# Kernel tuning notes

Measured on AMD Instinct MI355X. Metric: run time of the kernel, lower is better.

Reference implementation:

```python
import jax, jax.numpy as jnp
import numpy as np

NN_SIZE = 10  # matches init_kwargs nn_size


def _knn_idx(points, k):
    """points: (B,N,D). Returns (B,N,k) indices of k nearest neighbors, self excluded."""
    sq = jnp.sum(points * points, axis=-1)  # (B,N)
    # squared euclidean distances (B,N,N)
    d2 = sq[:, :, None] + sq[:, None, :] - 2.0 * jnp.einsum('bnd,bmd->bnm', points, points)
    _, idx = jax.lax.top_k(-d2, k + 1)  # smallest distances; first hit is self
    return idx[:, :, 1:]  # drop self -> (B,N,k)


def _uniform_laplacian(points, knn_idx):
    """points: (B,N,D); knn_idx: (B,N,K). lap = mean(neighbors) - point."""
    neigh = jax.vmap(lambda p, i: p[i])(points, knn_idx)  # (B,N,K,D) gather per batch
    return jnp.mean(neigh, axis=2) - points


def setup_inputs() -> dict:
    key = jax.random.key(0)
    k1, k2 = jax.random.split(key)
    B, N, D = 2, 8192, 3
    point1 = jax.random.normal(k1, (B, N, D), dtype=jnp.float32)
    point2 = jax.random.normal(k2, (B, N, D), dtype=jnp.float32)
    return {"point1": point1, "point2": point2}


def reference(point1, point2):
    knn_idx = _knn_idx(point1, NN_SIZE)          # connectivity from ref cloud
    lap1 = _uniform_laplacian(point1, knn_idx)   # (B,N,3)
    lap2 = _uniform_laplacian(point2, knn_idx)   # reuse knn_idx
    # metric = L1Loss (mean reduction); use_norm=False
    return jnp.mean(jnp.abs(lap1 - lap2))
```

## Files before the change

### kernel.cpp

```cpp
#include <hip/hip_runtime.h>
#include <math.h>


constexpr int NPTS  = 8192;
constexpr int NB    = 2;
constexpr int KNN   = 10;
constexpr int QPB   = 64;
constexpr int WPB   = 8;
constexpr int BLOCK = QPB * WPB;
constexpr int MASK13 = 0xFFFFE000;

constexpr int   G    = 32;
constexpr int   NC   = G * G * G;
constexpr float BMIN = -5.5f;
constexpr float BW   = 11.0f;
constexpr float H    = BW / G;
constexpr float INVH = (float)G / BW;

__device__ __forceinline__ void ins1(int l[KNN], int x) {
#pragma unroll
    for (int k = KNN - 1; k > 0; --k) l[k] = min(l[k], max(l[k - 1], x));
    l[0] = min(l[0], x);
}
__device__ __forceinline__ void ins2(int l[KNN], int a, int b) {
    const int b0 = min(a, b), b1 = max(a, b);
#pragma unroll
    for (int k = KNN - 1; k >= 2; --k)
        l[k] = min(l[k], min(max(l[k - 1], b0), max(l[k - 2], b1)));
    l[1] = min(l[1], min(max(l[0], b0), b1));
    l[0] = min(l[0], b0);
}
template<int S>
__device__ __forceinline__ void ins2s(int l[KNN], int a, int b) {
    const int b0 = min(a, b), b1 = max(a, b);
#pragma unroll
    for (int k = KNN - 1; k >= S + 2; --k)
        l[k] = min(l[k], min(max(l[k - 1], b0), max(l[k - 2], b1)));
    l[S + 1] = min(l[S + 1], min(max(l[S], b0), b1));
    l[S] = min(l[S], b0);
}
__device__ __forceinline__ void merge_sorted(int l[KNN], const int p[KNN]) {
    ins2s<0>(l, p[0], p[1]);
    ins2s<2>(l, p[2], p[3]);
    ins2s<4>(l, p[4], p[5]);
    ins2s<6>(l, p[6], p[7]);
    ins2s<8>(l, p[8], p[9]);
}

__global__ void pack_bin(const float* __restrict__ p1, float4* __restrict__ w,
                         int* __restrict__ hist, int* __restrict__ cellof) {
    const int i = blockIdx.x * blockDim.x + threadIdx.x;
    if (i >= NB * NPTS) return;
    const float x = p1[3 * i], y = p1[3 * i + 1], z = p1[3 * i + 2];
    w[i] = make_float4(x, y, z, fmaf(x, x, fmaf(y, y, z * z)));
    const int cx = min(max((int)floorf((x - BMIN) * INVH), 0), G - 1);
    const int cy = min(max((int)floorf((y - BMIN) * INVH), 0), G - 1);
    const int cz = min(max((int)floorf((z - BMIN) * INVH), 0), G - 1);
    const int c = (cz << 10) | (cy << 5) | cx;
    cellof[i] = c;
    atomicAdd(&hist[(i >> 13) * NC + c], 1);
}

__global__ __launch_bounds__(1024)
void scan_cells(const int* __restrict__ hist, int* __restrict__ starts,
                float* __restrict__ out, int* __restrict__ nfail) {
    __shared__ int wsum[16];
    const int b = blockIdx.x, t = threadIdx.x;
    if (b == 0 && t == 0) { out[0] = 0.0f; nfail[0] = 0; }
    const int* hb = hist + b * NC;
    int* sb = starts + b * (NC + 1);
    const int c0 = t * 32;
    int loc[32]; int sum = 0;
#pragma unroll
    for (int j = 0; j < 32; ++j) { loc[j] = hb[c0 + j]; sum += loc[j]; }
    const int lane = t & 63, wv = t >> 6;
    int incl = sum;
#pragma unroll
    for (int off = 1; off < 64; off <<= 1) {
        const int v = __shfl_up(incl, off);
        if (lane >= off) incl += v;
    }
    if (lane == 63) wsum[wv] = incl;
    __syncthreads();
    if (t < 16) {
        const int v = wsum[t];
        int iv = v;
#pragma unroll
        for (int off = 1; off < 16; off <<= 1) {
            const int u = __shfl_up(iv, off);
            if (t >= off) iv += u;
        }
        wsum[t] = iv - v;
    }
    __syncthreads();
    int run = wsum[wv] + incl - sum;
#pragma unroll
    for (int j = 0; j < 32; ++j) { sb[c0 + j] = run; run += loc[j]; }
    if (t == 1023) sb[NC] = run;
}

__global__ void scatter_all(const int* __restrict__ cellof,
                            const int* __restrict__ starts,
                            int* __restrict__ hist,
                            const float4* __restrict__ w,
                            const float* __restrict__ p2,
                            float4* __restrict__ wsorted,
                            float4* __restrict__ p2s) {
    const int i = blockIdx.x * blockDim.x + threadIdx.x;
    if (i >= NB * NPTS) return;
    const int b = i >> 13;
    const int c = cellof[i];
    const int old = atomicSub(&hist[b * NC + c], 1);
    const int pos = b * NPTS + starts[b * (NC + 1) + c] + old - 1;
    wsorted[pos] = w[i];
    p2s[pos] = make_float4(p2[3 * i], p2[3 * i + 1], p2[3 * i + 2], 0.0f);
}

template<int S>
__device__ __forceinline__ void scan_neigh(const float4* __restrict__ W,
                                           const int* __restrict__ st,
                                           int cx, int cy, int cz,
                                           float m2x, float m2y, float m2z,
                                           float q2, int qpos, int wv,
                                           int l[KNN])
{
    const int IMAX = 0x7FFFFFFF;
    constexpr int Wd = 2 * S + 1;
#pragma unroll
    for (int r = 0; r < Wd * Wd; ++r) {
        const int dy = r % Wd - S, dz = r / Wd - S;
        const int ay = cy + dy, az = cz + dz;
        int j0 = 0, j1 = 0;
        if ((unsigned)ay < G && (unsigned)az < G) {
            const int cbase = (az << 10) | (ay << 5);
            j0 = st[cbase + max(cx - S, 0)];
            j1 = st[cbase + min(cx + S, G - 1) + 1];
        }
        for (int j = j0 + wv; j < j1; j += WPB) {
            const float4 c4 = W[j];
            const float d2 = fmaf(m2x, c4.x,
                             fmaf(m2y, c4.y,
                             fmaf(m2z, c4.z, c4.w + q2)));
            int key = (__float_as_int(d2) & MASK13) | j;
            key = (j == qpos) ? IMAX : key;
            ins1(l, key);
        }
    }
}

__global__ __launch_bounds__(BLOCK)
void phase1(const float4* __restrict__ wsorted, const float4* __restrict__ p2s,
            const int* __restrict__ starts, float* __restrict__ out,
            int* __restrict__ nfail, int* __restrict__ worklist)
{
    __shared__ int mv[WPB * KNN * QPB];

    const int batch = blockIdx.x >> 7;
    const int lane  = threadIdx.x & 63;
    const int wv    = __builtin_amdgcn_readfirstlane(threadIdx.x >> 6);
    const int qpos  = ((blockIdx.x & 127) << 6) + lane;

    const float4* W  = wsorted + batch * NPTS;
    const float4* P2 = p2s + batch * NPTS;
    const int*    st = starts + batch * (NC + 1);

    const float4 qp = W[qpos];
    const int cx = min(max((int)floorf((qp.x - BMIN) * INVH), 0), G - 1);
    const int cy = min(max((int)floorf((qp.y - BMIN) * INVH), 0), G - 1);
    const int cz = min(max((int)floorf((qp.z - BMIN) * INVH), 0), G - 1);
    const float lox = BMIN + cx * H, loy = BMIN + cy * H, loz = BMIN + cz * H;
    const float df = fminf(fminf(fminf(qp.x - lox, lox + H - qp.x),
                                 fminf(qp.y - loy, loy + H - qp.y)),
                           fminf(qp.z - loz, loz + H - qp.z));
    const float m2x = -2.0f * qp.x, m2y = -2.0f * qp.y, m2z = -2.0f * qp.z;
    const float q2 = qp.w;
    const int IMAX = 0x7FFFFFFF;

    const bool sparse = __any(q2 > 4.8f);
    const int s = sparse ? 2 : 1;

    int l[KNN];
#pragma unroll
    for (int k = 0; k < KNN; ++k) l[k] = IMAX;

    if (sparse)
        scan_neigh<2>(W, st, cx, cy, cz, m2x, m2y, m2z, q2, qpos, wv, l);
    else
        scan_neigh<1>(W, st, cx, cy, cz, m2x, m2y, m2z, q2, qpos, wv, l);

#pragma unroll
    for (int k = 0; k < KNN; ++k) mv[(wv * KNN + k) * QPB + lane] = l[k];
    __syncthreads();

    if (threadIdx.x < QPB) {
        int M[KNN];
#pragma unroll
        for (int k = 0; k < KNN; ++k) M[k] = IMAX;
#pragma unroll
        for (int e = 0; e < WPB; ++e) {
            int p[KNN];
#pragma unroll
            for (int k = 0; k < KNN; ++k) p[k] = mv[(e * KNN + k) * QPB + lane];
            merge_sorted(M, p);
        }

        const float tau = __int_as_float(M[KNN - 1] & MASK13);
        const float R = (float)s * H + df;
        const bool covered = (tau <= R * R * 0.996f);
        float v = 0.0f;
        if (covered) {
            float s1x = 0, s1y = 0, s1z = 0, s2x = 0, s2y = 0, s2z = 0;
#pragma unroll
            for (int k = 0; k < KNN; ++k) {
                const int j = M[k] & (NPTS - 1);
                const float4 c4 = W[j];
                const float4 n2 = P2[j];
                s1x += c4.x; s1y += c4.y; s1z += c4.z;
                s2x += n2.x; s2y += n2.y; s2z += n2.z;
            }
            const float4 p2v = P2[qpos];
            const float dx = (s1x * 0.1f - qp.x) - (s2x * 0.1f - p2v.x);
            const float dy2 = (s1y * 0.1f - qp.y) - (s2y * 0.1f - p2v.y);
            const float dz2 = (s1z * 0.1f - qp.z) - (s2z * 0.1f - p2v.z);
            v = fabsf(dx) + fabsf(dy2) + fabsf(dz2);
        } else {
            const int wi = atomicAdd(nfail, 1);
            worklist[wi] = (batch << 16) | qpos;
        }
#pragma unroll
        for (int off = 32; off >= 1; off >>= 1) v += __shfl_down(v, off);
        if (threadIdx.x == 0)
            atomicAdd(out, v * (1.0f / (float)(NB * NPTS * 3)));
    }
}

constexpr int P2BLK = 256;
constexpr int P2GRID = 512;

__global__ __launch_bounds__(P2BLK)
void phase2(const float4* __restrict__ wsorted, const float4* __restrict__ p2s,
            const int* __restrict__ nfail, const int* __restrict__ worklist,
            float* __restrict__ out)
{
    const int lane = threadIdx.x & 63;
    const int wv   = threadIdx.x >> 6;
    const int wid  = blockIdx.x * (P2BLK / 64) + wv;
    const int NW   = P2GRID * (P2BLK / 64);
    const int nf   = *nfail;
    const int IMAX = 0x7FFFFFFF;
    float acc = 0.0f;

    for (int i = wid; i < nf; i += NW) {
        const int e = worklist[i];
        const int batch = e >> 16, qpos = e & 0xFFFF;
        const float4* W  = wsorted + batch * NPTS;
        const float4* P2 = p2s + batch * NPTS;
        const float4 qp = W[qpos];
        const float m2x = -2.0f * qp.x, m2y = -2.0f * qp.y, m2z = -2.0f * qp.z;
        const float q2 = qp.w;

        int l[KNN];
#pragma unroll
        for (int k = 0; k < KNN; ++k) l[k] = IMAX;

#pragma unroll 2
        for (int it = 0; it < NPTS / 128; ++it) {
            const int ja = it * 128 + lane, jb = ja + 64;
            const float4 ca = W[ja];
            const float4 cb = W[jb];
            const float da = fmaf(m2x, ca.x, fmaf(m2y, ca.y, fmaf(m2z, ca.z, ca.w + q2)));
            const float db = fmaf(m2x, cb.x, fmaf(m2y, cb.y, fmaf(m2z, cb.z, cb.w + q2)));
            int ka = (__float_as_int(da) & MASK13) | ja;
            int kb = (__float_as_int(db) & MASK13) | jb;
            ka = (ja == qpos) ? IMAX : ka;
            kb = (jb == qpos) ? IMAX : kb;
            ins2(l, ka, kb);
        }
        for (int off = 1; off < 64; off <<= 1) {
            int p[KNN];
#pragma unroll
            for (int k = 0; k < KNN; ++k) p[k] = __shfl_xor(l[k], off);
            merge_sorted(l, p);
        }
        float s1x = 0, s1y = 0, s1z = 0, s2x = 0, s2y = 0, s2z = 0;
#pragma unroll
        for (int k = 0; k < KNN; ++k) {
            const int j = l[k] & (NPTS - 1);
            const float4 c4 = W[j];
            const float4 n2 = P2[j];
            s1x += c4.x; s1y += c4.y; s1z += c4.z;
            s2x += n2.x; s2y += n2.y; s2z += n2.z;
        }
        const float4 p2v = P2[qpos];
        const float dx = (s1x * 0.1f - qp.x) - (s2x * 0.1f - p2v.x);
        const float dy = (s1y * 0.1f - qp.y) - (s2y * 0.1f - p2v.y);
        const float dz = (s1z * 0.1f - qp.z) - (s2z * 0.1f - p2v.z);
        if (lane == 0) acc += fabsf(dx) + fabsf(dy) + fabsf(dz);
    }

    if (lane == 0 && acc != 0.0f)
        atomicAdd(out, acc * (1.0f / (float)(NB * NPTS * 3)));
}

constexpr int CHUNK = NPTS / WPB;

__global__ void prep_pack(const float* __restrict__ p, float4* __restrict__ w) {
    const int i = blockIdx.x * blockDim.x + threadIdx.x;
    if (i < NB * NPTS) {
        const float x = p[3 * i], y = p[3 * i + 1], z = p[3 * i + 2];
        w[i] = make_float4(x, y, z, fmaf(x, x, fmaf(y, y, z * z)));
    }
}

__global__ __launch_bounds__(BLOCK, 2)
void knn_lap(const float4* __restrict__ w1, const float* __restrict__ p2,
             float* __restrict__ out)
{
    __shared__ int mv[WPB * KNN * QPB];
    const int batch = blockIdx.x >> 7;
    const int qbase = (blockIdx.x & 127) << 6;
    const int lane  = threadIdx.x & 63;
    const int wv    = __builtin_amdgcn_readfirstlane(threadIdx.x >> 6);
    const int query = qbase + lane;
    const float4* Wb = w1 + batch * NPTS;
    const float4 qp = Wb[query];
    const float m2x = -2.0f * qp.x, m2y = -2.0f * qp.y, m2z = -2.0f * qp.z;
    const float q2 = qp.w;
    const int IMAX = 0x7FFFFFFF;
    int l[KNN];
#pragma unroll
    for (int k = 0; k < KNN; ++k) l[k] = IMAX;
    const int c0 = wv * CHUNK;
    const float4* cand = Wb + c0;
#pragma unroll 4
    for (int i = 0; i < CHUNK; i += 2) {
        const float4 ca = cand[i];
        const float4 cb = cand[i + 1];
        const int ja = c0 + i, jb = ja + 1;
        const float da = fmaf(m2x, ca.x, fmaf(m2y, ca.y, fmaf(m2z, ca.z, ca.w + q2)));
        const float db = fmaf(m2x, cb.x, fmaf(m2y, cb.y, fmaf(m2z, cb.z, cb.w + q2)));
        int ka = (__float_as_int(da) & MASK13) | ja;
        int kb = (__float_as_int(db) & MASK13) | jb;
        ka = (ja == query) ? IMAX : ka;
        kb = (jb == query) ? IMAX : kb;
        ins2(l, ka, kb);
    }
#pragma unroll
    for (int k = 0; k < KNN; ++k) mv[(wv * KNN + k) * QPB + lane] = l[k];
    __syncthreads();
    if (threadIdx.x < QPB) {
        int m[KNN];
#pragma unroll
        for (int k = 0; k < KNN; ++k) m[k] = IMAX;
#pragma unroll
        for (int e = 0; e < WPB; ++e) {
            int p[KNN];
#pragma unroll
            for (int k = 0; k < KNN; ++k) p[k] = mv[(e * KNN + k) * QPB + lane];
            merge_sorted(m, p);
        }
        const float* P2b = p2 + (size_t)batch * NPTS * 3;
        float s1x = 0, s1y = 0, s1z = 0, s2x = 0, s2y = 0, s2z = 0;
#pragma unroll
        for (int k = 0; k < KNN; ++k) {
            const int j = m[k] & (NPTS - 1);
            const float4 c = Wb[j];
            s1x += c.x; s1y += c.y; s1z += c.z;
            s2x += P2b[3 * j + 0]; s2y += P2b[3 * j + 1]; s2z += P2b[3 * j + 2];
        }
        const int q = qbase + threadIdx.x;
        const float p2x = P2b[3 * q + 0], p2y = P2b[3 * q + 1], p2z = P2b[3 * q + 2];
        const float dx = (s1x * 0.1f - qp.x) - (s2x * 0.1f - p2x);
        const float dy = (s1y * 0.1f - qp.y) - (s2y * 0.1f - p2y);
        const float dz = (s1z * 0.1f - qp.z) - (s2z * 0.1f - p2z);
        float v = fabsf(dx) + fabsf(dy) + fabsf(dz);
#pragma unroll
        for (int off = 32; off >= 1; off >>= 1) v += __shfl_down(v, off);
        if (threadIdx.x == 0)
            atomicAdd(out, v * (1.0f / (float)(NB * NPTS * 3)));
    }
}

extern "C" void kernel_launch(void* const* d_in, const int* in_sizes, int n_in,
                              void* d_out, int out_size, void* d_ws, size_t ws_size,
                              hipStream_t stream) {
    const float* p1 = (const float*)d_in[0];
    const float* p2 = (const float*)d_in[1];
    float* out = (float*)d_out;

    size_t off = 0;
    float4* w       = (float4*)d_ws;               off += (size_t)NB * NPTS * 16;
    int*    hist    = (int*)((char*)d_ws + off);   off += (size_t)NB * NC * 4;
    int*    starts  = (int*)((char*)d_ws + off);   off += (size_t)NB * (NC + 1) * 4 + 8;
    int*    cellof  = (int*)((char*)d_ws + off);   off += (size_t)NB * NPTS * 4;
    float4* wsorted = (float4*)((char*)d_ws + off); off += (size_t)NB * NPTS * 16;
    float4* p2s     = (float4*)((char*)d_ws + off); off += (size_t)NB * NPTS * 16;
    int*    nfail   = (int*)((char*)d_ws + off);   off += 16;
    int*    worklist= (int*)((char*)d_ws + off);   off += (size_t)NB * NPTS * 4;

    if (ws_size < off) {
        hipMemsetAsync(out, 0, sizeof(float), stream);
        prep_pack<<<(NB * NPTS + 255) / 256, 256, 0, stream>>>(p1, w);
        knn_lap<<<NB * (NPTS / QPB), BLOCK, 0, stream>>>(w, p2, out);
        return;
    }

    hipMemsetAsync(hist, 0, (size_t)NB * NC * 4, stream);
    pack_bin<<<(NB * NPTS + 255) / 256, 256, 0, stream>>>(p1, w, hist, cellof);
    scan_cells<<<NB, 1024, 0, stream>>>(hist, starts, out, nfail);
    scatter_all<<<(NB * NPTS + 255) / 256, 256, 0, stream>>>(cellof, starts, hist,
                                                             w, p2, wsorted, p2s);
    phase1<<<NB * (NPTS / QPB), BLOCK, 0, stream>>>(wsorted, p2s, starts, out,
                                                    nfail, worklist);
    phase2<<<P2GRID, P2BLK, 0, stream>>>(wsorted, p2s, nfail, worklist, out);
}
```

Measured before the change: 142.0 us.

## Widen phase1 to 16 waves per query block and prefetch grid candidates

Phase1 now uses 16 waves per block of 64 queries, so each query's cell scan is split across more waves. The per-row cell-range loads are hoisted into arrays before the scan, and each candidate is software-prefetched one stride ahead. The sparse/dense search radius is now picked per lane instead of per wave, and the output/nfail reset moves from scan_cells into pack_bin. The trade-offs are more shared-memory merge work, per-lane branch divergence inside a wave, and a larger block that may lower occupancy.

```diff
diff --git a/kernel.cpp b/kernel.cpp
--- a/kernel.cpp
+++ b/kernel.cpp
@@ -6,7 +6,7 @@
 constexpr int NB    = 2;
 constexpr int KNN   = 10;
 constexpr int QPB   = 64;
-constexpr int WPB   = 8;
+constexpr int WPB   = 16;
 constexpr int BLOCK = QPB * WPB;
 constexpr int MASK13 = 0xFFFFE000;
 
@@ -48,9 +48,11 @@
 }
 
 __global__ void pack_bin(const float* __restrict__ p1, float4* __restrict__ w,
-                         int* __restrict__ hist, int* __restrict__ cellof) {
+                         int* __restrict__ hist, int* __restrict__ cellof,
+                         float* __restrict__ out, int* __restrict__ nfail) {
     const int i = blockIdx.x * blockDim.x + threadIdx.x;
     if (i >= NB * NPTS) return;
+    if (i == 0) { out[0] = 0.0f; nfail[0] = 0; }
     const float x = p1[3 * i], y = p1[3 * i + 1], z = p1[3 * i + 2];
     w[i] = make_float4(x, y, z, fmaf(x, x, fmaf(y, y, z * z)));
     const int cx = min(max((int)floorf((x - BMIN) * INVH), 0), G - 1);
@@ -62,25 +64,23 @@
 }
 
 __global__ __launch_bounds__(1024)
-void scan_cells(const int* __restrict__ hist, int* __restrict__ starts,
-                float* __restrict__ out, int* __restrict__ nfail) {
+void scan_cells(const int* __restrict__ hist, int* __restrict__ starts) {
     __shared__ int wsum[16];
     const int b = blockIdx.x, t = threadIdx.x;
-    if (b == 0 && t == 0) { out[0] = 0.0f; nfail[0] = 0; }
     const int* hb = hist + b * NC;
     int* sb = starts + b * (NC + 1);
     const int c0 = t * 32;
     int loc[32]; int sum = 0;
 #pragma unroll
     for (int j = 0; j < 32; ++j) { loc[j] = hb[c0 + j]; sum += loc[j]; }
-    const int lane = t & 63, wv = t >> 6;
+    const int lane = t & 63, wvi = t >> 6;
     int incl = sum;
 #pragma unroll
     for (int off = 1; off < 64; off <<= 1) {
         const int v = __shfl_up(incl, off);
         if (lane >= off) incl += v;
     }
-    if (lane == 63) wsum[wv] = incl;
+    if (lane == 63) wsum[wvi] = incl;
     __syncthreads();
     if (t < 16) {
         const int v = wsum[t];
@@ -93,7 +93,7 @@
         wsum[t] = iv - v;
     }
     __syncthreads();
-    int run = wsum[wv] + incl - sum;
+    int run = wsum[wvi] + incl - sum;
 #pragma unroll
     for (int j = 0; j < 32; ++j) { sb[c0 + j] = run; run += loc[j]; }
     if (t == 1023) sb[NC] = run;
@@ -117,33 +117,48 @@
 }
 
 template<int S>
-__device__ __forceinline__ void scan_neigh(const float4* __restrict__ W,
-                                           const int* __restrict__ st,
-                                           int cx, int cy, int cz,
-                                           float m2x, float m2y, float m2z,
-                                           float q2, int qpos, int wv,
-                                           int l[KNN])
+__device__ __forceinline__ void scan_batched(const float4* __restrict__ W,
+                                             const int* __restrict__ st,
+                                             int cx, int cy, int cz,
+                                             float m2x, float m2y, float m2z,
+                                             float q2, int qpos, int wv,
+                                             int l[KNN])
 {
+    constexpr int Wd = 2 * S + 1;
+    constexpr int R  = Wd * Wd;
     const int IMAX = 0x7FFFFFFF;
-    constexpr int Wd = 2 * S + 1;
-#pragma unroll
-    for (int r = 0; r < Wd * Wd; ++r) {
+    int J0[R], J1[R];
+#pragma unroll
+    for (int r = 0; r < R; ++r) {
         const int dy = r % Wd - S, dz = r / Wd - S;
         const int ay = cy + dy, az = cz + dz;
-        int j0 = 0, j1 = 0;
-        if ((unsigned)ay < G && (unsigned)az < G) {
-            const int cbase = (az << 10) | (ay << 5);
-            j0 = st[cbase + max(cx - S, 0)];
-            j1 = st[cbase + min(cx + S, G - 1) + 1];
-        }
-        for (int j = j0 + wv; j < j1; j += WPB) {
-            const float4 c4 = W[j];
-            const float d2 = fmaf(m2x, c4.x,
-                             fmaf(m2y, c4.y,
-                             fmaf(m2z, c4.z, c4.w + q2)));
-            int key = (__float_as_int(d2) & MASK13) | j;
-            key = (j == qpos) ? IMAX : key;
-            ins1(l, key);
+        const bool ok = ((unsigned)ay < G) && ((unsigned)az < G);
+        const int cbase = (az << 10) | (ay << 5);
+        const int lo = cbase + max(cx - S, 0);
+        const int hi = cbase + min(cx + S, G - 1) + 1;
+        J0[r] = ok ? st[lo] : 0;
+        J1[r] = ok ? st[hi] : 0;
+    }
+#pragma unroll
+    for (int r = 0; r < R; ++r) {
+        const int j1 = J1[r];
+        int j = J0[r] + wv;
+        if (j < j1) {
+            float4 c4 = W[j];
+            while (true) {
+                const int jn = j + WPB;
+                const bool more = jn < j1;
+                float4 nx;
+                if (more) nx = W[jn];
+                const float d2 = fmaf(m2x, c4.x,
+                                 fmaf(m2y, c4.y,
+                                 fmaf(m2z, c4.z, c4.w + q2)));
+                int key = (__float_as_int(d2) & MASK13) | j;
+                key = (j == qpos) ? IMAX : key;
+                ins1(l, key);
+                if (!more) break;
+                c4 = nx; j = jn;
+            }
         }
     }
 }
@@ -176,17 +191,16 @@
     const float q2 = qp.w;
     const int IMAX = 0x7FFFFFFF;
 
-    const bool sparse = __any(q2 > 4.8f);
-    const int s = sparse ? 2 : 1;
+    const int sCov = (q2 > 4.8f) ? 2 : 1;
 
     int l[KNN];
 #pragma unroll
     for (int k = 0; k < KNN; ++k) l[k] = IMAX;
 
-    if (sparse)
-        scan_neigh<2>(W, st, cx, cy, cz, m2x, m2y, m2z, q2, qpos, wv, l);
+    if (sCov == 1)
+        scan_batched<1>(W, st, cx, cy, cz, m2x, m2y, m2z, q2, qpos, wv, l);
     else
-        scan_neigh<1>(W, st, cx, cy, cz, m2x, m2y, m2z, q2, qpos, wv, l);
+        scan_batched<2>(W, st, cx, cy, cz, m2x, m2y, m2z, q2, qpos, wv, l);
 
 #pragma unroll
     for (int k = 0; k < KNN; ++k) mv[(wv * KNN + k) * QPB + lane] = l[k];
@@ -205,7 +219,7 @@
         }
 
         const float tau = __int_as_float(M[KNN - 1] & MASK13);
-        const float R = (float)s * H + df;
+        const float R = (float)sCov * H + df;
         const bool covered = (tau <= R * R * 0.996f);
         float v = 0.0f;
         if (covered) {
@@ -302,7 +316,9 @@
         atomicAdd(out, acc * (1.0f / (float)(NB * NPTS * 3)));
 }
 
-constexpr int CHUNK = NPTS / WPB;
+constexpr int FB_WPB = 8;
+constexpr int FB_BLOCK = QPB * FB_WPB;
+constexpr int CHUNK = NPTS / FB_WPB;
 
 __global__ void prep_pack(const float* __restrict__ p, float4* __restrict__ w) {
     const int i = blockIdx.x * blockDim.x + threadIdx.x;
@@ -312,11 +328,11 @@
     }
 }
 
-__global__ __launch_bounds__(BLOCK, 2)
+__global__ __launch_bounds__(FB_BLOCK, 2)
 void knn_lap(const float4* __restrict__ w1, const float* __restrict__ p2,
              float* __restrict__ out)
 {
-    __shared__ int mv[WPB * KNN * QPB];
+    __shared__ int mv[FB_WPB * KNN * QPB];
     const int batch = blockIdx.x >> 7;
     const int qbase = (blockIdx.x & 127) << 6;
     const int lane  = threadIdx.x & 63;
@@ -353,7 +369,7 @@
 #pragma unroll
         for (int k = 0; k < KNN; ++k) m[k] = IMAX;
 #pragma unroll
-        for (int e = 0; e < WPB; ++e) {
+        for (int e = 0; e < FB_WPB; ++e) {
             int p[KNN];
 #pragma unroll
             for (int k = 0; k < KNN; ++k) p[k] = mv[(e * KNN + k) * QPB + lane];
@@ -401,13 +417,14 @@
     if (ws_size < off) {
         hipMemsetAsync(out, 0, sizeof(float), stream);
         prep_pack<<<(NB * NPTS + 255) / 256, 256, 0, stream>>>(p1, w);
-        knn_lap<<<NB * (NPTS / QPB), BLOCK, 0, stream>>>(w, p2, out);
+        knn_lap<<<NB * (NPTS / QPB), FB_BLOCK, 0, stream>>>(w, p2, out);
         return;
     }
 
     hipMemsetAsync(hist, 0, (size_t)NB * NC * 4, stream);
-    pack_bin<<<(NB * NPTS + 255) / 256, 256, 0, stream>>>(p1, w, hist, cellof);
-    scan_cells<<<NB, 1024, 0, stream>>>(hist, starts, out, nfail);
+    pack_bin<<<(NB * NPTS + 255) / 256, 256, 0, stream>>>(p1, w, hist, cellof,
+                                                          out, nfail);
+    scan_cells<<<NB, 1024, 0, stream>>>(hist, starts);
     scatter_all<<<(NB * NPTS + 255) / 256, 256, 0, stream>>>(cellof, starts, hist,
                                                              w, p2, wsorted, p2s);
     phase1<<<NB * (NPTS / QPB), BLOCK, 0, stream>>>(wsorted, p2s, starts, out,
```

Result: faster. 120.9 us (-14.9%).
